# Optimization experiments

Hardware: AMD Instinct MI355X
Metric: run time of the kernel (lower is better)

The kernel has to match this reference:

```python
import jax, jax.numpy as jnp
import numpy as np

BATCH = 2048
N_CHANS = 128
SUBDIM = 64
N_OUT = 4
KARCHER_STEPS = 2
TRACE_EPS = 1e-4
REEIG_THR = 1e-4
BN_EPS = 1e-5
SQRT2 = float(np.sqrt(2.0))


def _sym(X):
    return 0.5 * (X + jnp.swapaxes(X, -1, -2))


def _fapply(X, fn):
    # apply fn to eigenvalues of a batch of symmetric matrices
    w, V = jnp.linalg.eigh(X)
    return jnp.einsum('...ij,...j,...kj->...ik', V, fn(w), V)


def spd_logm(X):
    return _fapply(X, jnp.log)


def spd_expm(X):
    return _fapply(X, jnp.exp)


def spd_powm(X, p):
    return _fapply(X, lambda w: jnp.exp(p * jnp.log(w)))


def setup_inputs() -> dict:
    key = jax.random.key(0)
    k1, k2, k3 = jax.random.split(key, 3)
    # SPD covariance inputs: Wishart-style, eigenvalues distinct a.s.
    A = jax.random.normal(k1, (BATCH, N_CHANS, 2 * N_CHANS), jnp.float32)
    X = A @ jnp.swapaxes(A, -1, -2) / (2 * N_CHANS) + 1e-3 * jnp.eye(N_CHANS, dtype=jnp.float32)
    # BiMap weight: stiefel (semi-orthogonal) init
    W = jnp.linalg.qr(jax.random.normal(k2, (N_CHANS, SUBDIM), jnp.float32))[0]
    L = SUBDIM * (SUBDIM + 1) // 2  # 2080
    Wc = jax.random.normal(k3, (N_OUT, L), jnp.float32) * 0.02
    bc = jnp.zeros((N_OUT,), jnp.float32)
    # BN bias SPD param: near identity but with distinct eigenvalues (keeps eigh grad finite)
    bn_bias = jnp.diag(jnp.linspace(0.9, 1.1, SUBDIM, dtype=jnp.float32))
    return dict(X=X, alpha=jnp.zeros((), jnp.float32), W=W,
                bn_gamma=jnp.ones((), jnp.float32), bn_bias=bn_bias, Wc=Wc, bc=bc)


def reference(X, alpha, W, bn_gamma, bn_bias, Wc, bc):
    n = X.shape[-1]
    I_n = jnp.eye(n, dtype=X.dtype)
    # TraceNorm: normalize to (approximately) unit trace
    tr = jnp.trace(X, axis1=-2, axis2=-1)[:, None, None]
    X = X / (tr + TRACE_EPS)
    # Shrinkage: (1-a) X + a * (tr(X)/n) I, learnable a (init 0)
    mu = jnp.trace(X, axis1=-2, axis2=-1)[:, None, None] / n
    X = (1.0 - alpha) * X + alpha * mu * I_n
    # BiMap: W^T X W  -> (B, d, d)
    X = _sym(jnp.einsum('ji,bjk,kl->bil', W, X, W))
    # ReEig: clamp eigenvalues at threshold
    X = _fapply(X, lambda w: jnp.maximum(w, REEIG_THR))
    # SPDBatchNormMeanVar (training mode, batch stats):
    # Karcher mean G (log-Euclidean init + Karcher flow steps)
    G = spd_expm(jnp.mean(spd_logm(X), axis=0))
    for _ in range(KARCHER_STEPS):
        Gs = spd_powm(G, 0.5)
        Gi = spd_powm(G, -0.5)
        G = Gs @ spd_expm(jnp.mean(spd_logm(_sym(Gi @ X @ Gi)), axis=0)) @ Gs
        G = _sym(G)
    Gi = spd_powm(G, -0.5)
    Lt = spd_logm(_sym(Gi @ X @ Gi))            # tangent vectors at identity
    v = jnp.mean(jnp.sum(Lt * Lt, axis=(-2, -1)))  # batch dispersion
    Y = spd_expm(Lt * (bn_gamma / jnp.sqrt(v + BN_EPS)))
    # affine bias: congruence with SPD bias param
    Bs = spd_powm(_sym(bn_bias), 0.5)
    Y = _sym(Bs @ Y @ Bs)
    # LogEig + upper-triangle vectorization (off-diag * sqrt(2))
    Lg = spd_logm(Y)
    d = Y.shape[-1]
    iu, ju = jnp.triu_indices(d)
    coef = jnp.where(iu == ju, 1.0, SQRT2).astype(X.dtype)
    vec = Lg[:, iu, ju] * coef                   # (B, d(d+1)/2)
    return vec @ Wc.T + bc
```

## Files before the change

kernel.cpp:

```cpp
#include <hip/hip_runtime.h>
#include <math.h>


#define NS_HI   5
#define NSC_IT  12
#define C1      0.0038729833f
#define LNC1    (-5.553730f)
#define SPLIT_S 4096.f
#define SPLIT_R (1.f/4096.f)

typedef _Float16 h16;
typedef _Float16 h16x8 __attribute__((ext_vector_type(8)));
typedef _Float16 h16x4 __attribute__((ext_vector_type(4)));
typedef float    f32x4 __attribute__((ext_vector_type(4)));

#define WS_S1   ((size_t)0)
#define WS_R2   ((size_t)8388608)
#define WS_SM   ((size_t)16777216)
#define SM_LBAR  0
#define SM_EBAR1 4096
#define SM_EBAR2 8192
#define SM_GI0   12288
#define SM_GS0   16384
#define SM_GI1   20480
#define SM_GS1   24576
#define SM_GI2   28672
#define SM_GS2   32768
#define SM_BS    36864
#define SM_VPART 40960
#define SM_S     40992

__device__ __forceinline__ float4 ld4(const float* p){ return *(const float4*)p; }
__device__ __forceinline__ void  st4(float* p, float4 v){ *(float4*)p = v; }

__device__ __forceinline__ int eoff(int r, int c){ return (r*128 + c*2) ^ ((r&7)<<4); }

__device__ __forceinline__ h16x8 frag_ld(const h16* p, int row, int ks, int lg){
  int off = (row*128 + ks*64 + lg*16) ^ ((row&7)<<4);
  return *(const h16x8*)((const char*)p + off);
}
__device__ __forceinline__ h16x8 frag_ld2(const h16* p, int row, int ks, int lg){
  int off = (row*256 + ks*64 + lg*16) ^ ((row&7)<<4);
  return *(const h16x8*)((const char*)p + off);
}
__device__ __forceinline__ h16x4 h4_ld(const h16* p, int r, int c4){
  return *(const h16x4*)((const char*)p + eoff(r,c4));
}
__device__ __forceinline__ void h4_st(h16* p, int r, int c4, h16x4 v){
  *(h16x4*)((char*)p + eoff(r,c4)) = v;
}
__device__ __forceinline__ void split2(float v, h16& h, h16& l){
  h16 hh = (h16)v;
  h = hh;
  l = (h16)((v - (float)hh) * SPLIT_S);
}
__device__ __forceinline__ float join2(h16 h, h16 l){
  return (float)h + (float)l * SPLIT_R;
}

template<int AS,int BS,int GP>
__device__ __forceinline__ void mmT(const h16* Lh,const h16* Ll,
                                    const h16* Rh,const h16* Rl,const h16* gR,
                                    f32x4 acc[2][2], int lane,int wv){
  const int lr=lane&15, lg=lane>>4;
  const int rb=(wv&1)*32, cb=(wv>>1)*32;
  h16x8 ah[2][2], al[2][2];
  #pragma unroll
  for(int rt=0;rt<2;rt++){
    #pragma unroll
    for(int ks=0;ks<2;ks++){
      ah[rt][ks]=frag_ld(Lh, rb+16*rt+lr, ks, lg);
      if(AS) al[rt][ks]=frag_ld(Ll, rb+16*rt+lr, ks, lg);
    }
  }
  f32x4 aM[2][2], aC[2][2];
  const f32x4 vz={0.f,0.f,0.f,0.f};
  #pragma unroll
  for(int rt=0;rt<2;rt++){ aM[rt][0]=vz; aM[rt][1]=vz; aC[rt][0]=vz; aC[rt][1]=vz; }
  #pragma unroll
  for(int ct=0;ct<2;ct++){
    #pragma unroll
    for(int ks=0;ks<2;ks++){
      h16x8 bh, bl;
      if(GP){
        const h16* g = gR + (cb+16*ct+lr)*64 + ks*32 + lg*8;
        bh = *(const h16x8*)g;
        if(BS) bl = *(const h16x8*)(g+4096);
      }else{
        bh = frag_ld(Rh, cb+16*ct+lr, ks, lg);
        if(BS) bl = frag_ld(Rl, cb+16*ct+lr, ks, lg);
      }
      #pragma unroll
      for(int rt=0;rt<2;rt++){
        aM[rt][ct]=__builtin_amdgcn_mfma_f32_16x16x32_f16(ah[rt][ks],bh,aM[rt][ct],0,0,0);
        if(AS) aC[rt][ct]=__builtin_amdgcn_mfma_f32_16x16x32_f16(al[rt][ks],bh,aC[rt][ct],0,0,0);
        if(BS) aC[rt][ct]=__builtin_amdgcn_mfma_f32_16x16x32_f16(ah[rt][ks],bl,aC[rt][ct],0,0,0);
      }
    }
  }
  #pragma unroll
  for(int rt=0;rt<2;rt++)
    #pragma unroll
    for(int ct=0;ct<2;ct++)
      acc[rt][ct] = (AS||BS) ? (aM[rt][ct] + aC[rt][ct]*SPLIT_R) : aM[rt][ct];
}

__device__ __forceinline__ void stS(h16* Dh,h16* Dl,const f32x4 acc[2][2],
                                    const float (*dI)[2][4],
                                    int lane,int wv,float scale,float dadd){
  const int lr=lane&15, lg=lane>>4, rb=(wv&1)*32, cb=(wv>>1)*32;
  #pragma unroll
  for(int rt=0;rt<2;rt++){
    int i0=rb+16*rt+lg*4;
    #pragma unroll
    for(int ct=0;ct<2;ct++){
      int j=cb+16*ct+lr;
      h16x4 h4,l4;
      #pragma unroll
      for(int r=0;r<4;r++){
        float x=fmaf(acc[rt][ct][r],scale, dadd*dI[rt][ct][r]);
        h16 hh,ll; split2(x,hh,ll); h4[r]=hh; l4[r]=ll;
      }
      int off=(j*128+i0*2)^((j&7)<<4);
      *(h16x4*)((char*)Dh+off)=h4;
      *(h16x4*)((char*)Dl+off)=l4;
    }
  }
}
__device__ __forceinline__ void stH(h16* Dh,const f32x4 acc[2][2],
                                    const float (*dI)[2][4],
                                    int lane,int wv,float scale,float dadd){
  const int lr=lane&15, lg=lane>>4, rb=(wv&1)*32, cb=(wv>>1)*32;
  #pragma unroll
  for(int rt=0;rt<2;rt++){
    int i0=rb+16*rt+lg*4;
    #pragma unroll
    for(int ct=0;ct<2;ct++){
      int j=cb+16*ct+lr;
      h16x4 h4;
      #pragma unroll
      for(int r=0;r<4;r++){
        float x=fmaf(acc[rt][ct][r],scale, dadd*dI[rt][ct][r]);
        h4[r]=(h16)x;
      }
      int off=(j*128+i0*2)^((j&7)<<4);
      *(h16x4*)((char*)Dh+off)=h4;
    }
  }
}

__device__ __forceinline__ void st_gl(float* G, const f32x4 acc[2][2],
                                      int lane,int wv,float scale,float dadd){
  const int lr=lane&15, lg=lane>>4, rb=(wv&1)*32, cb=(wv>>1)*32;
  #pragma unroll
  for(int rt=0;rt<2;rt++){
    int i0=rb+16*rt+lg*4;
    #pragma unroll
    for(int ct=0;ct<2;ct++){
      int j=cb+16*ct+lr;
      float4 v; float* vf=(float*)&v;
      #pragma unroll
      for(int r=0;r<4;r++){
        float x=acc[rt][ct][r]*scale;
        if (i0+r==j) x += dadd;
        vf[r]=x;
      }
      st4(G + j*64 + i0, v);
    }
  }
}

__device__ __forceinline__ void st_park(h16* gh, const f32x4 acc[2][2], int lane,int wv){
  const int lr=lane&15, lg=lane>>4, rb=(wv&1)*32, cb=(wv>>1)*32;
  #pragma unroll
  for(int rt=0;rt<2;rt++){
    int i0=rb+16*rt+lg*4;
    #pragma unroll
    for(int ct=0;ct<2;ct++){
      int j=cb+16*ct+lr;
      h16x4 h4,l4;
      #pragma unroll
      for(int r=0;r<4;r++){ h16 hh,ll; split2(acc[rt][ct][r],hh,ll); h4[r]=hh; l4[r]=ll; }
      *(h16x4*)(gh + j*64 + i0) = h4;
      *(h16x4*)(gh + 4096 + j*64 + i0) = l4;
    }
  }
}

__device__ __forceinline__ void snap(const h16* Ph,const h16* Pl,float (*v)[2][4],
                                     int lane,int wv){
  const int lr=lane&15, lg=lane>>4, rb=(wv&1)*32, cb=(wv>>1)*32;
  #pragma unroll
  for(int rt=0;rt<2;rt++){
    int i0=rb+16*rt+lg*4;
    #pragma unroll
    for(int ct=0;ct<2;ct++){
      int j=cb+16*ct+lr;
      h16x4 h=h4_ld(Ph,j,i0), l=h4_ld(Pl,j,i0);
      #pragma unroll
      for(int r=0;r<4;r++) v[rt][ct][r]=join2(h[r],l[r]);
    }
  }
}

__device__ __forceinline__ void fill_gl(h16* Ph, h16* Pl, const float* g,
                                        float scale, float dshift, int tid){
  int r = tid>>2;
  #pragma unroll
  for(int q=0;q<4;q++){
    int c4 = (tid&3)*16 + q*4;
    float4 v = ld4(g + r*64 + c4);
    float vv[4]={v.x,v.y,v.z,v.w};
    h16x4 h4,l4;
    #pragma unroll
    for(int j=0;j<4;j++){
      float x = vv[j];
      if (c4+j == r) x += dshift;
      x *= scale;
      h16 hh,ll; split2(x,hh,ll); h4[j]=hh; l4[j]=ll;
    }
    h4_st(Ph,r,c4,h4); h4_st(Pl,r,c4,l4);
  }
}

__device__ __forceinline__ void plane_out(const h16* Ph, const h16* Pl, float* g,
                                          float scale, int tid){
  int r=tid>>2;
  #pragma unroll
  for(int q=0;q<4;q++){
    int c4=(tid&3)*16+q*4;
    h16x4 h4=h4_ld(Ph,r,c4), l4=h4_ld(Pl,r,c4);
    float4 v;
    v.x=join2(h4[0],l4[0])*scale;
    v.y=join2(h4[1],l4[1])*scale;
    v.z=join2(h4[2],l4[2])*scale;
    v.w=join2(h4[3],l4[3])*scale;
    st4(g + r*64 + c4, v);
  }
}

__device__ __forceinline__ void diag_add(h16* Ph, h16* Pl, float add, int tid){
  if (tid<64){
    int off = (tid*128 + tid*2) ^ ((tid&7)<<4);
    h16* ph = (h16*)((char*)Ph + off);
    h16* pl = (h16*)((char*)Pl + off);
    float v = join2(*ph,*pl) + add;
    h16 hh,ll; split2(v,hh,ll);
    *ph=hh; *pl=ll;
  }
}

__device__ float block_sum(float v, float* red, int tid){
  red[tid]=v; __syncthreads();
  for(int off=128; off>0; off>>=1){
    if (tid<off) red[tid]+=red[tid+off];
    __syncthreads();
  }
  float r=red[0]; __syncthreads();
  return r;
}

__device__ __forceinline__ float cfj(int j, int J){
  return (j<=J)? 1.f/(float)(2*j+1) : 0.f;
}

__device__ void ns_inv3(h16* Ah,h16* Al,h16* Xh,h16* Xl,h16* Th,h16* Tl,
                        float* red,const float (*dI)[2][4],
                        int tid,int lane,int wv,float lminB){
  {
    int row=tid>>2, seg=tid&3;
    float s=0.f;
    #pragma unroll
    for(int q=0;q<4;q++){
      h16x4 h4 = h4_ld(Ah,row,seg*16+q*4);
      #pragma unroll
      for(int j=0;j<4;j++) s += fabsf((float)h4[j]);
    }
    red[tid]=s*1.001f; __syncthreads();
    if((tid&3)==0) red[tid]=red[tid]+red[tid+1]+red[tid+2]+red[tid+3];
    __syncthreads();
    if(tid==0){ float m=0.f; for(int i=0;i<64;i++) m=fmaxf(m,red[4*i]); red[0]=m; }
    __syncthreads();
  }
  float alpha = 2.f/(lminB + red[0]);
  {
    int r=tid>>2;
    h16 ahh,all_; split2(alpha,ahh,all_);
    #pragma unroll
    for(int q=0;q<4;q++){
      int c4=(tid&3)*16+q*4;
      h16x4 h4={(h16)0,(h16)0,(h16)0,(h16)0};
      h16x4 l4={(h16)0,(h16)0,(h16)0,(h16)0};
      #pragma unroll
      for(int j=0;j<4;j++) if (c4+j==r){ h4[j]=ahh; l4[j]=all_; }
      h4_st(Xh,r,c4,h4); h4_st(Xl,r,c4,l4);
    }
  }
  __syncthreads();
  f32x4 acc[2][2];
  for(int it=0;it<NS_HI;it++){
    mmT<0,0,0>(Ah,0,Xh,0,0,acc,lane,wv); __syncthreads();
    stH(Th,acc,dI,lane,wv,-1.f,2.f); __syncthreads();
    mmT<0,0,0>(Xh,0,Th,0,0,acc,lane,wv); __syncthreads();
    stH(Xh,acc,dI,lane,wv,1.f,0.f); __syncthreads();
  }
  mmT<1,0,0>(Ah,Al,Xh,0,0,acc,lane,wv); __syncthreads();
  stS(Th,Tl,acc,dI,lane,wv,-1.f,2.f); __syncthreads();
  mmT<0,1,0>(Xh,0,Th,Tl,0,acc,lane,wv); __syncthreads();
  stS(Xh,Xl,acc,dI,lane,wv,1.f,0.f); __syncthreads();
  mmT<1,1,0>(Ah,Al,Xh,Xl,0,acc,lane,wv); __syncthreads();
  stS(Th,Tl,acc,dI,lane,wv,-1.f,2.f); __syncthreads();
  mmT<1,1,0>(Xh,Xl,Th,Tl,0,acc,lane,wv); __syncthreads();
  stS(Xh,Xl,acc,dI,lane,wv,1.f,0.f); __syncthreads();
}

__device__ void logm3(h16* Ah,h16* Al,h16* Xh,h16* Xl,h16* Th,h16* Tl,
                      h16* parkh, float* red, const float (*dI)[2][4],
                      float cshift,int C,int J,int tid,int lane,int wv,
                      f32x4 accOut[2][2]){
  ns_inv3(Ah,Al,Xh,Xl,Th,Tl,red,dI,tid,lane,wv,cshift);
  diag_add(Ah,Al,-2.f*cshift,tid);
  __syncthreads();
  f32x4 acc[2][2];
  mmT<1,1,0>(Ah,Al,Xh,Xl,0,acc,lane,wv); __syncthreads();
  stS(Th,Tl,acc,dI,lane,wv,1.f,0.f);
  st_park(parkh,acc,lane,wv);
  __syncthreads();
  mmT<1,1,0>(Th,Tl,Th,Tl,0,acc,lane,wv); __syncthreads();
  stS(Ah,Al,acc,dI,lane,wv,1.f,0.f); __syncthreads();
  mmT<1,1,0>(Ah,Al,Ah,Al,0,acc,lane,wv); __syncthreads();
  stS(Xh,Xl,acc,dI,lane,wv,1.f,0.f); __syncthreads();
  float sv[2][2][4], s2v[2][2][4];
  f32x4 accw[2][2];
  mmT<1,1,0>(Xh,Xl,Ah,Al,0,accw,lane,wv);
  snap(Ah,Al,sv,lane,wv);
  snap(Xh,Xl,s2v,lane,wv);
  {
    float a0=cfj(3*C-3,J),a1=cfj(3*C-2,J),a2=cfj(3*C-1,J);
    int r=tid>>2;
    #pragma unroll
    for(int q=0;q<4;q++){
      int c4=(tid&3)*16+q*4;
      h16x4 sh=h4_ld(Ah,r,c4), sl=h4_ld(Al,r,c4);
      h16x4 th=h4_ld(Xh,r,c4), tl=h4_ld(Xl,r,c4);
      h16x4 h4,l4;
      #pragma unroll
      for(int jj=0;jj<4;jj++){
        float v=a1*join2(sh[jj],sl[jj])+a2*join2(th[jj],tl[jj]);
        if(c4+jj==r) v+=a0;
        h16 hh,ll; split2(v,hh,ll); h4[jj]=hh; l4[jj]=ll;
      }
      h4_st(Th,r,c4,h4); h4_st(Tl,r,c4,l4);
    }
  }
  __syncthreads();
  stS(Xh,Xl,accw,dI,lane,wv,1.f,0.f); __syncthreads();
  for(int i=C-2;i>=0;i--){
    mmT<1,1,0>(Th,Tl,Xh,Xl,0,acc,lane,wv);
    float a0=cfj(3*i,J),a1=cfj(3*i+1,J),a2=cfj(3*i+2,J);
    #pragma unroll
    for(int rt=0;rt<2;rt++)
      #pragma unroll
      for(int ct=0;ct<2;ct++)
        #pragma unroll
        for(int r=0;r<4;r++)
          acc[rt][ct][r]+=a0*dI[rt][ct][r]+a1*sv[rt][ct][r]+a2*s2v[rt][ct][r];
    __syncthreads();
    stS(Th,Tl,acc,dI,lane,wv,1.f,0.f);
    __syncthreads();
  }
  mmT<1,1,1>(Th,Tl,(const h16*)0,(const h16*)0,parkh,accOut,lane,wv);
}

__device__ void exp3(h16* Lh,h16* Ll, h16* Bh,h16* Bl, h16* Ph,h16* Pl,
                     const float (*dI)[2][4], float s,
                     int tid,int lane,int wv){
  f32x4 acc[2][2];
  mmT<1,1,0>(Lh,Ll,Lh,Ll,0,acc,lane,wv); __syncthreads();
  stS(Bh,Bl,acc,dI,lane,wv,1.f,0.f); __syncthreads();
  float lv[2][2][4], l2v[2][2][4];
  snap(Lh,Ll,lv,lane,wv);
  snap(Bh,Bl,l2v,lane,wv);
  float aj[15]; aj[0]=1.f;
  #pragma unroll
  for(int j=1;j<15;j++) aj[j]=aj[j-1]*s/(float)j;
  {
    int r=tid>>2;
    #pragma unroll
    for(int q=0;q<4;q++){
      int c4=(tid&3)*16+q*4;
      h16x4 sh=h4_ld(Lh,r,c4), sl=h4_ld(Ll,r,c4);
      h16x4 th=h4_ld(Bh,r,c4), tl=h4_ld(Bl,r,c4);
      h16x4 h4,l4;
      #pragma unroll
      for(int jj=0;jj<4;jj++){
        float v = aj[13]*join2(sh[jj],sl[jj]) + aj[14]*join2(th[jj],tl[jj]);
        if (c4+jj==r) v+=aj[12];
        h16 hh,ll; split2(v,hh,ll); h4[jj]=hh; l4[jj]=ll;
      }
      h4_st(Ph,r,c4,h4); h4_st(Pl,r,c4,l4);
    }
  }
  __syncthreads();
  mmT<1,1,0>(Bh,Bl,Lh,Ll,0,acc,lane,wv); __syncthreads();
  stS(Bh,Bl,acc,dI,lane,wv,1.f,0.f); __syncthreads();
  #pragma unroll
  for(int i=3;i>=0;i--){
    mmT<1,1,0>(Ph,Pl,Bh,Bl,0,acc,lane,wv);
    #pragma unroll
    for(int rt=0;rt<2;rt++)
      #pragma unroll
      for(int ct=0;ct<2;ct++)
        #pragma unroll
        for(int r=0;r<4;r++)
          acc[rt][ct][r]+=aj[3*i]*dI[rt][ct][r]+aj[3*i+1]*lv[rt][ct][r]+aj[3*i+2]*l2v[rt][ct][r];
    __syncthreads();
    stS(Ph,Pl,acc,dI,lane,wv,1.f,0.f);
    __syncthreads();
  }
}

__device__ void ns_sqrt3(h16* Yh,h16* Yl,h16* Zh,h16* Zl,h16* Th,h16* Tl,
                         const float (*dI)[2][4], int tid,int lane,int wv){
  {
    int r=tid>>2;
    h16 oh,ol; split2(1.f,oh,ol);
    #pragma unroll
    for(int q=0;q<4;q++){
      int c4=(tid&3)*16+q*4;
      h16x4 h4={(h16)0,(h16)0,(h16)0,(h16)0};
      h16x4 l4={(h16)0,(h16)0,(h16)0,(h16)0};
      #pragma unroll
      for(int j=0;j<4;j++) if (c4+j==r){ h4[j]=oh; l4[j]=ol; }
      h4_st(Zh,r,c4,h4); h4_st(Zl,r,c4,l4);
    }
  }
  __syncthreads();
  f32x4 aY[2][2], aZ[2][2];
  for(int it=0; it<NSC_IT; it++){
    mmT<1,1,0>(Zh,Zl,Yh,Yl,0,aY,lane,wv); __syncthreads();
    stS(Th,Tl,aY,dI,lane,wv,-0.5f,1.5f); __syncthreads();
    mmT<1,1,0>(Yh,Yl,Th,Tl,0,aY,lane,wv);
    mmT<1,1,0>(Th,Tl,Zh,Zl,0,aZ,lane,wv);
    __syncthreads();
    stS(Yh,Yl,aY,dI,lane,wv,1.f,0.f);
    stS(Zh,Zl,aZ,dI,lane,wv,1.f,0.f);
    __syncthreads();
  }
}

#define DECL_DI(dIname) \
  float dIname[2][2][4]; \
  { int rb_=(wv&1)*32, cb_=(wv>>1)*32; \
    _Pragma("unroll") \
    for(int rt=0;rt<2;rt++) \
      _Pragma("unroll") \
      for(int ct=0;ct<2;ct++) \
        _Pragma("unroll") \
        for(int r=0;r<4;r++) \
          dIname[rt][ct][r]=((rb_+16*rt+(lane>>4)*4+r)==(cb_+16*ct+(lane&15)))?1.f:0.f; }


__global__ __launch_bounds__(256) void kA(const float* __restrict__ Xg, const float* alphaP,
    const float* __restrict__ Wg, float* S1g, float* R2){
  __shared__ __align__(16) char lds[65536];
  int tid=threadIdx.x, b=blockIdx.x, lane=tid&63, wv=tid>>6;
  int lr=lane&15, lg=lane>>4;
  DECL_DI(dI);
  const float* Xb = Xg + (size_t)b*16384;
  h16* Wph=(h16*)lds;         h16* Wpl=Wph+8192;
  h16* Tph=(h16*)(lds+32768); h16* Tpl=Tph+8192;
  {
    int k0=tid>>1, nh=(tid&1)*32;
    const float* wr = Wg + k0*64 + nh;
    #pragma unroll
    for(int q=0;q<8;q++){
      float4 u=ld4(wr+q*4);
      float uu[4]={u.x,u.y,u.z,u.w};
      #pragma unroll
      for(int j=0;j<4;j++){
        int n=nh+q*4+j;
        h16 hh,ll; split2(uu[j],hh,ll);
        int off=(n*256+k0*2)^((n&7)<<4);
        *(h16*)((char*)Wph+off)=hh;
        *(h16*)((char*)Wpl+off)=ll;
      }
    }
  }
  float tv=(tid<128)? Xb[tid*129]:0.f;
  float tr=block_sum(tv,(float*)(lds+32768),tid);
  float al=alphaP[0];
  float f1=1.f/(tr+1e-4f);
  float scl=(1.f-al)*f1;
  float shift=al*(tr*f1)*(1.f/128.f);
  f32x4 aM[2][4], aC[2][4];
  const f32x4 vz={0.f,0.f,0.f,0.f};
  #pragma unroll
  for(int rt=0;rt<2;rt++)
    #pragma unroll
    for(int ct=0;ct<4;ct++){ aM[rt][ct]=vz; aC[rt][ct]=vz; }
  int mb=wv*32;
  for(int ks=0;ks<4;ks++){
    h16x8 xah[2], xal[2];
    #pragma unroll
    for(int rt=0;rt<2;rt++){
      const float* px=Xb+(size_t)(mb+16*rt+lr)*128+ks*32+lg*8;
      float4 u0=ld4(px), u1=ld4(px+4);
      float uv[8]={u0.x,u0.y,u0.z,u0.w,u1.x,u1.y,u1.z,u1.w};
      #pragma unroll
      for(int e=0;e<8;e++){ h16 hh,ll; split2(uv[e],hh,ll); xah[rt][e]=hh; xal[rt][e]=ll; }
    }
    #pragma unroll
    for(int ct=0;ct<4;ct++){
      h16x8 bh=frag_ld2(Wph,ct*16+lr,ks,lg);
      h16x8 bl=frag_ld2(Wpl,ct*16+lr,ks,lg);
      #pragma unroll
      for(int rt=0;rt<2;rt++){
        aM[rt][ct]=__builtin_amdgcn_mfma_f32_16x16x32_f16(xah[rt],bh,aM[rt][ct],0,0,0);
        aC[rt][ct]=__builtin_amdgcn_mfma_f32_16x16x32_f16(xal[rt],bh,aC[rt][ct],0,0,0);
        aC[rt][ct]=__builtin_amdgcn_mfma_f32_16x16x32_f16(xah[rt],bl,aC[rt][ct],0,0,0);
      }
    }
  }
  __syncthreads();
  #pragma unroll
  for(int rt=0;rt<2;rt++){
    int i0=mb+16*rt+lg*4;
    #pragma unroll
    for(int ct=0;ct<4;ct++){
      int j=ct*16+lr;
      h16x4 h4,l4;
      #pragma unroll
      for(int r=0;r<4;r++){
        float x=aM[rt][ct][r]+aC[rt][ct][r]*SPLIT_R;
        h16 hh,ll; split2(x,hh,ll); h4[r]=hh; l4[r]=ll;
      }
      int off=(j*256+i0*2)^((j&7)<<4);
      *(h16x4*)((char*)Tph+off)=h4;
      *(h16x4*)((char*)Tpl+off)=l4;
    }
  }
  __syncthreads();
  f32x4 sM[2][2], sC[2][2];
  #pragma unroll
  for(int rt=0;rt<2;rt++){ sM[rt][0]=vz; sM[rt][1]=vz; sC[rt][0]=vz; sC[rt][1]=vz; }
  int rb=(wv&1)*32, cb=(wv>>1)*32;
  for(int ks=0;ks<4;ks++){
    h16x8 ah2[2], al2[2];
    #pragma unroll
    for(int rt=0;rt<2;rt++){
      ah2[rt]=frag_ld2(Wph,rb+16*rt+lr,ks,lg);
      al2[rt]=frag_ld2(Wpl,rb+16*rt+lr,ks,lg);
    }
    #pragma unroll
    for(int ct=0;ct<2;ct++){
      h16x8 bh=frag_ld2(Tph,cb+16*ct+lr,ks,lg);
      h16x8 bl=frag_ld2(Tpl,cb+16*ct+lr,ks,lg);
      #pragma unroll
      for(int rt=0;rt<2;rt++){
        sM[rt][ct]=__builtin_amdgcn_mfma_f32_16x16x32_f16(ah2[rt],bh,sM[rt][ct],0,0,0);
        sC[rt][ct]=__builtin_amdgcn_mfma_f32_16x16x32_f16(al2[rt],bh,sC[rt][ct],0,0,0);
        sC[rt][ct]=__builtin_amdgcn_mfma_f32_16x16x32_f16(ah2[rt],bl,sC[rt][ct],0,0,0);
      }
    }
  }
  f32x4 accS[2][2];
  #pragma unroll
  for(int rt=0;rt<2;rt++)
    #pragma unroll
    for(int ct=0;ct<2;ct++) accS[rt][ct]=sM[rt][ct]+sC[rt][ct]*SPLIT_R;
  __syncthreads();
  st_gl(S1g+(size_t)b*4096, accS, lane,wv, scl, shift);
  h16* Ah=(h16*)lds;          h16* Al=Ah+4096;
  h16* Xh=(h16*)(lds+16384);  h16* Xl=Xh+4096;
  h16* Th=(h16*)(lds+32768);  h16* Tl=Th+4096;
  float* red=(float*)(lds+49152);
  stS(Ah,Al,accS,dI,lane,wv, scl, shift + C1);
  __syncthreads();
  f32x4 aL[2][2];
  h16* parkh=(h16*)(R2+(size_t)b*4096);
  logm3(Ah,Al,Xh,Xl,Th,Tl,parkh,red,dI, C1, 11, 30, tid,lane,wv, aL);
  __syncthreads();
  st_gl(R2+(size_t)b*4096, aL, lane,wv, 2.f, LNC1);
}

__global__ __launch_bounds__(256) void kRed(const float* __restrict__ R2, float* outM, float scale){
  __shared__ float red[256];
  int tid=threadIdx.x; int ee=tid&31; int sl=tid>>5;
  int e0 = blockIdx.x*32 + ee;
  float s=0.f;
  for(int j=0;j<256;j++) s += R2[(size_t)(sl+8*j)*4096 + e0];
  red[tid]=s; __syncthreads();
  if (sl<4) red[tid]+=red[tid+128];
  __syncthreads();
  if (sl<2) red[tid]+=red[tid+64];
  __syncthreads();
  if (sl==0) outM[e0] = (red[tid]+red[tid+32])*scale;
}

__global__ __launch_bounds__(256) void kB(const float* Lbar, const float* biasP,
     float* Gi0, float* Gs0, float* Bs){
  __shared__ __align__(16) char lds[50176];
  int tid=threadIdx.x, lane=tid&63, wv=tid>>6;
  DECL_DI(dI);
  h16* s0h=(h16*)lds;          h16* s0l=s0h+4096;
  h16* s1h=(h16*)(lds+16384);  h16* s1l=s1h+4096;
  h16* s2h=(h16*)(lds+32768);  h16* s2l=s2h+4096;
  float* red=(float*)(lds+49152);
  float tr = block_sum((tid<64)? Lbar[tid*65]:0.f, red, tid);
  float cb_ = tr*(1.f/64.f);
  fill_gl(s0h,s0l, Lbar, 0.5f, -cb_, tid);
  __syncthreads();
  exp3(s0h,s0l,s1h,s1l,s2h,s2l, dI, 1.f, tid,lane,wv);
  plane_out(s2h,s2l, Gs0, expf(0.5f*cb_), tid);
  __syncthreads();
  exp3(s0h,s0l,s1h,s1l,s2h,s2l, dI, -1.f, tid,lane,wv);
  plane_out(s2h,s2l, Gi0, expf(-0.5f*cb_), tid);
  __syncthreads();
  float tb = block_sum((tid<64)? biasP[tid*65]:0.f, red, tid);
  float itb=1.f/tb;
  {
    int r=tid>>2;
    #pragma unroll
    for(int q=0;q<4;q++){
      int c4=(tid&3)*16+q*4;
      float4 v=ld4(biasP + r*64 + c4);
      float vv[4]={v.x,v.y,v.z,v.w};
      h16x4 h4,l4;
      #pragma unroll
      for(int j=0;j<4;j++){
        float x = 0.5f*(vv[j] + biasP[(c4+j)*64 + r]) * itb;
        h16 hh,ll; split2(x,hh,ll); h4[j]=hh; l4[j]=ll;
      }
      h4_st(s0h,r,c4,h4); h4_st(s0l,r,c4,l4);
    }
  }
  __syncthreads();
  ns_sqrt3(s0h,s0l,s1h,s1l,s2h,s2l, dI, tid,lane,wv);
  plane_out(s0h,s0l, Bs, sqrtf(tb), tid);
}

__global__ __launch_bounds__(256,3) void kC(const float* __restrict__ S1g, const float* GiP,
     float* R2, float* vpart, int doV){
  __shared__ __align__(16) char lds[50176];
  int tid=threadIdx.x, b=blockIdx.x, lane=tid&63, wv=tid>>6;
  DECL_DI(dI);
  h16* s0h=(h16*)lds;          h16* s0l=s0h+4096;
  h16* s1h=(h16*)(lds+16384);  h16* s1l=s1h+4096;
  h16* s2h=(h16*)(lds+32768);  h16* s2l=s2h+4096;
  float* red=(float*)(lds+49152);
  fill_gl(s0h,s0l, S1g+(size_t)b*4096, 1.f,0.f, tid);
  fill_gl(s1h,s1l, GiP, 1.f,0.f, tid);
  __syncthreads();
  f32x4 acc[2][2];
  mmT<1,1,0>(s0h,s0l,s1h,s1l,0,acc,lane,wv); __syncthreads();
  stS(s2h,s2l,acc,dI,lane,wv,1.f,0.f); __syncthreads();
  mmT<1,1,0>(s1h,s1l,s2h,s2l,0,acc,lane,wv); __syncthreads();
  stS(s0h,s0l,acc,dI,lane,wv,1.f,1.f); __syncthreads();
  f32x4 aL[2][2];
  h16* parkh=(h16*)(R2+(size_t)b*4096);
  logm3(s0h,s0l,s1h,s1l,s2h,s2l,parkh,red,dI, 1.f, 11, 30, tid,lane,wv, aL);
  __syncthreads();
  st_gl(R2+(size_t)b*4096, aL, lane,wv, 2.f, 0.f);
  if (doV){
    float s=0.f;
    #pragma unroll
    for(int rt=0;rt<2;rt++)
      #pragma unroll
      for(int ct=0;ct<2;ct++)
        #pragma unroll
        for(int r=0;r<4;r++){ float lv=2.f*aL[rt][ct][r]; s=fmaf(lv,lv,s); }
    __syncthreads();
    s = block_sum(s, red, tid);
    if (tid==0) atomicAdd(vpart + (b&31), s);
  }
}

__global__ __launch_bounds__(256) void kD(const float* Ebar, const float* GsP,
     float* GsN, float* GiN){
  __shared__ __align__(16) char lds[50176];
  int tid=threadIdx.x, lane=tid&63, wv=tid>>6;
  DECL_DI(dI);
  h16* s0h=(h16*)lds;          h16* s0l=s0h+4096;
  h16* s1h=(h16*)(lds+16384);  h16* s1l=s1h+4096;
  h16* s2h=(h16*)(lds+32768);  h16* s2l=s2h+4096;
  float* red=(float*)(lds+49152);
  fill_gl(s0h,s0l, Ebar, 1.f,0.f, tid); __syncthreads();
  exp3(s0h,s0l,s1h,s1l,s2h,s2l, dI, 1.f, tid,lane,wv);
  fill_gl(s0h,s0l, GsP, 1.f,0.f, tid);
  __syncthreads();
  f32x4 acc[2][2];
  mmT<1,1,0>(s2h,s2l,s0h,s0l,0,acc,lane,wv); __syncthreads();
  stS(s1h,s1l,acc,dI,lane,wv,1.f,0.f); __syncthreads();
  mmT<1,1,0>(s0h,s0l,s1h,s1l,0,acc,lane,wv);
  float tv=0.f;
  #pragma unroll
  for(int rt=0;rt<2;rt++)
    #pragma unroll
    for(int ct=0;ct<2;ct++)
      #pragma unroll
      for(int r=0;r<4;r++) tv += acc[rt][ct][r]*dI[rt][ct][r];
  float t = block_sum(tv, red, tid);
  stS(s0h,s0l,acc,dI,lane,wv,1.f/t,0.f); __syncthreads();
  ns_sqrt3(s0h,s0l,s1h,s1l,s2h,s2l, dI, tid,lane,wv);
  float st_=sqrtf(t), ist=1.f/st_;
  plane_out(s0h,s0l, GsN, st_, tid);
  plane_out(s1h,s1l, GiN, ist, tid);
}

__global__ void kF2(const float* vpart, const float* gammaP, float* sOut){
  if (threadIdx.x==0 && blockIdx.x==0){
    float v=0.f;
    for(int i=0;i<32;i++) v+=vpart[i];
    v *= (1.f/2048.f);
    sOut[0] = gammaP[0] / sqrtf(v + 1e-5f);
  }
}

__global__ __launch_bounds__(256,3) void kG(float* R2, const float* BsP, const float* sP,
     const float* __restrict__ WcP, const float* bcP, float* outP){
  __shared__ __align__(16) char lds[50176];
  int tid=threadIdx.x, b=blockIdx.x, lane=tid&63, wv=tid>>6;
  DECL_DI(dI);
  h16* s0h=(h16*)lds;          h16* s0l=s0h+4096;
  h16* s1h=(h16*)(lds+16384);  h16* s1l=s1h+4096;
  h16* s2h=(h16*)(lds+32768);  h16* s2l=s2h+4096;
  float* red=(float*)(lds+49152);
  fill_gl(s0h,s0l, R2+(size_t)b*4096, 1.f,0.f, tid); __syncthreads();
  float s = sP[0];
  exp3(s0h,s0l,s1h,s1l,s2h,s2l, dI, s, tid,lane,wv);
  fill_gl(s0h,s0l, BsP, 1.f,0.f, tid);
  __syncthreads();
  f32x4 acc[2][2];
  mmT<1,1,0>(s2h,s2l,s0h,s0l,0,acc,lane,wv); __syncthreads();
  stS(s1h,s1l,acc,dI,lane,wv,1.f,0.f); __syncthreads();
  mmT<1,1,0>(s0h,s0l,s1h,s1l,0,acc,lane,wv); __syncthreads();
  stS(s2h,s2l,acc,dI,lane,wv,1.f,1.f); __syncthreads();
  f32x4 aL[2][2];
  h16* parkh=(h16*)(R2+(size_t)b*4096);
  logm3(s2h,s2l,s0h,s0l,s1h,s1l,parkh,red,dI, 1.f, 6, 15, tid,lane,wv, aL);
  float o0=0,o1=0,o2=0,o3=0;
  {
    int lr=lane&15, lq=lane>>4, rb=(wv&1)*32, cb=(wv>>1)*32;
    #pragma unroll
    for(int rt=0;rt<2;rt++)
      #pragma unroll
      for(int ct=0;ct<2;ct++)
        #pragma unroll
        for(int r=0;r<4;r++){
          int i=rb+16*rt+lq*4+r, j=cb+16*ct+lr;
          float lg2=2.f*aL[rt][ct][r];
          int a=(i<j)? i:j, bb=(i<j)? j:i;
          int tri = a*64 - ((a*(a-1))>>1) + (bb-a);
          float w = (i==j)? lg2 : lg2*0.70710678118654752f;
          o0=fmaf(w, WcP[tri],      o0);
          o1=fmaf(w, WcP[2080+tri], o1);
          o2=fmaf(w, WcP[4160+tri], o2);
          o3=fmaf(w, WcP[6240+tri], o3);
        }
  }
  __syncthreads();
  float* redv=(float*)lds;
  float4 pk; pk.x=o0; pk.y=o1; pk.z=o2; pk.w=o3;
  st4(redv+4*tid, pk); __syncthreads();
  for(int off=128; off>0; off>>=1){
    if (tid<off){
      float4 x=ld4(redv+4*tid), y=ld4(redv+4*(tid+off));
      x.x+=y.x; x.y+=y.y; x.z+=y.z; x.w+=y.w;
      st4(redv+4*tid, x);
    }
    __syncthreads();
  }
  if (tid==0){
    outP[b*4+0]=redv[0]+bcP[0];
    outP[b*4+1]=redv[1]+bcP[1];
    outP[b*4+2]=redv[2]+bcP[2];
    outP[b*4+3]=redv[3]+bcP[3];
  }
}

extern "C" void kernel_launch(void* const* d_in, const int* in_sizes, int n_in,
                              void* d_out, int out_size, void* d_ws, size_t ws_size,
                              hipStream_t stream){
  const float* X     = (const float*)d_in[0];
  const float* alpha = (const float*)d_in[1];
  const float* W     = (const float*)d_in[2];
  const float* gamma = (const float*)d_in[3];
  const float* bias  = (const float*)d_in[4];
  const float* Wc    = (const float*)d_in[5];
  const float* bc    = (const float*)d_in[6];
  float* ws = (float*)d_ws;
  float* S1 = ws + WS_S1;
  float* R2 = ws + WS_R2;
  float* sm = ws + WS_SM;

  hipMemsetAsync(sm + SM_VPART, 0, 33*sizeof(float), stream);

  kA  <<<2048,256,0,stream>>>(X, alpha, W, S1, R2);
  kRed<<<128, 256,0,stream>>>(R2, sm+SM_LBAR, 1.f/2048.f);
  kB  <<<1,   256,0,stream>>>(sm+SM_LBAR, bias, sm+SM_GI0, sm+SM_GS0, sm+SM_BS);
  kC  <<<2048,256,0,stream>>>(S1, sm+SM_GI0, R2, nullptr, 0);
  kRed<<<128, 256,0,stream>>>(R2, sm+SM_EBAR1, 1.f/2048.f);
  kD  <<<1,   256,0,stream>>>(sm+SM_EBAR1, sm+SM_GS0, sm+SM_GS1, sm+SM_GI1);
  kC  <<<2048,256,0,stream>>>(S1, sm+SM_GI1, R2, nullptr, 0);
  kRed<<<128, 256,0,stream>>>(R2, sm+SM_EBAR2, 1.f/2048.f);
  kD  <<<1,   256,0,stream>>>(sm+SM_EBAR2, sm+SM_GS1, sm+SM_GS2, sm+SM_GI2);
  kC  <<<2048,256,0,stream>>>(S1, sm+SM_GI2, R2, sm+SM_VPART, 1);
  kF2 <<<1,1,0,stream>>>(sm+SM_VPART, gamma, sm+SM_S);
  kG  <<<2048,256,0,stream>>>(R2, sm+SM_BS, sm+SM_S, Wc, bc, (float*)d_out);
}
```

Before: 923.1 us.

## Restructure matrix log/exp polynomial evaluation with degree-4 Paterson-Stockmeyer and ping-pong buffers

Replaces the degree-3 block Horner evaluation in the matrix logarithm with a degree-4 Paterson-Stockmeyer scheme that uses register-held powers. The series term counts are retuned per call site (fewer Chebyshev/atanh terms for the first logm), and the final Newton-Schulz refinement step is dropped in one case. Ping-pong LDS buffers let one barrier per step be removed in the Newton-Schulz and Horner loops, and the high-precision low halves of the early Newton-Schulz iterates are no longer kept. exp is restructured the same way, and the inverse exponential is computed from a negated input. The aim is fewer matmuls and fewer syncs, at the risk of reduced accuracy from the shorter series and the skipped refinement.

```diff
diff --git a/kernel.cpp b/kernel.cpp
--- a/kernel.cpp
+++ b/kernel.cpp
@@ -2,7 +2,6 @@
 #include <math.h>
 
 
-#define NS_HI   5
 #define NSC_IT  12
 #define C1      0.0038729833f
 #define LNC1    (-5.553730f)
@@ -203,6 +202,40 @@
   }
 }
 
+__device__ __forceinline__ void snapa(float (*v)[2][4], const f32x4 acc[2][2]){
+  #pragma unroll
+  for(int rt=0;rt<2;rt++)
+    #pragma unroll
+    for(int ct=0;ct<2;ct++)
+      #pragma unroll
+      for(int r=0;r<4;r++) v[rt][ct][r]=acc[rt][ct][r];
+}
+
+__device__ __forceinline__ void addK4(f32x4 acc[2][2], const float (*dI)[2][4],
+    const float (*sv)[2][4], const float (*s2v)[2][4], const float (*s3v)[2][4],
+    float a0,float a1,float a2,float a3){
+  #pragma unroll
+  for(int rt=0;rt<2;rt++)
+    #pragma unroll
+    for(int ct=0;ct<2;ct++)
+      #pragma unroll
+      for(int r=0;r<4;r++)
+        acc[rt][ct][r] += a0*dI[rt][ct][r] + a1*sv[rt][ct][r]
+                        + a2*s2v[rt][ct][r] + a3*s3v[rt][ct][r];
+}
+
+__device__ __forceinline__ void addK3(f32x4 acc[2][2], const float (*dI)[2][4],
+    const float (*lv)[2][4], const float (*l2v)[2][4],
+    float a0,float a1,float a2){
+  #pragma unroll
+  for(int rt=0;rt<2;rt++)
+    #pragma unroll
+    for(int ct=0;ct<2;ct++)
+      #pragma unroll
+      for(int r=0;r<4;r++)
+        acc[rt][ct][r] += a0*dI[rt][ct][r] + a1*lv[rt][ct][r] + a2*l2v[rt][ct][r];
+}
+
 __device__ __forceinline__ void fill_gl(h16* Ph, h16* Pl, const float* g,
                                         float scale, float dshift, int tid){
   int r = tid>>2;
@@ -264,9 +297,10 @@
   return (j<=J)? 1.f/(float)(2*j+1) : 0.f;
 }
 
-__device__ void ns_inv3(h16* Ah,h16* Al,h16* Xh,h16* Xl,h16* Th,h16* Tl,
+template<int NSS>
+__device__ void ns_inv4(h16* Ah,h16* Al,h16* Xh,h16* Xl,h16* Th,h16* Tl,
                         float* red,const float (*dI)[2][4],
-                        int tid,int lane,int wv,float lminB){
+                        int tid,int lane,int wv,float lminB,float postshift){
   {
     int row=tid>>2, seg=tid&3;
     float s=0.f;
@@ -285,137 +319,124 @@
   float alpha = 2.f/(lminB + red[0]);
   {
     int r=tid>>2;
-    h16 ahh,all_; split2(alpha,ahh,all_);
+    h16 ahh=(h16)alpha;
     #pragma unroll
     for(int q=0;q<4;q++){
       int c4=(tid&3)*16+q*4;
       h16x4 h4={(h16)0,(h16)0,(h16)0,(h16)0};
-      h16x4 l4={(h16)0,(h16)0,(h16)0,(h16)0};
-      #pragma unroll
-      for(int j=0;j<4;j++) if (c4+j==r){ h4[j]=ahh; l4[j]=all_; }
-      h4_st(Xh,r,c4,h4); h4_st(Xl,r,c4,l4);
+      #pragma unroll
+      for(int j=0;j<4;j++) if (c4+j==r) h4[j]=ahh;
+      h4_st(Xh,r,c4,h4);
     }
   }
   __syncthreads();
   f32x4 acc[2][2];
-  for(int it=0;it<NS_HI;it++){
-    mmT<0,0,0>(Ah,0,Xh,0,0,acc,lane,wv); __syncthreads();
-    stH(Th,acc,dI,lane,wv,-1.f,2.f); __syncthreads();
-    mmT<0,0,0>(Xh,0,Th,0,0,acc,lane,wv); __syncthreads();
-    stH(Xh,acc,dI,lane,wv,1.f,0.f); __syncthreads();
-  }
-  mmT<1,0,0>(Ah,Al,Xh,0,0,acc,lane,wv); __syncthreads();
+  #pragma unroll
+  for(int it=0;it<5;it++){
+    const h16* Xa=(it&1)?Xl:Xh;
+    h16* Ta=(it&1)?Tl:Th;
+    h16* Xn=(it&1)?Xh:Xl;
+    mmT<0,0,0>(Ah,0,Xa,0,0,acc,lane,wv);
+    stH(Ta,acc,dI,lane,wv,-1.f,2.f); __syncthreads();
+    mmT<0,0,0>(Xa,0,Ta,0,0,acc,lane,wv);
+    stH(Xn,acc,dI,lane,wv,1.f,0.f); __syncthreads();
+  }
+  mmT<1,0,0>(Ah,Al,Xl,0,0,acc,lane,wv);
   stS(Th,Tl,acc,dI,lane,wv,-1.f,2.f); __syncthreads();
-  mmT<0,1,0>(Xh,0,Th,Tl,0,acc,lane,wv); __syncthreads();
-  stS(Xh,Xl,acc,dI,lane,wv,1.f,0.f); __syncthreads();
-  mmT<1,1,0>(Ah,Al,Xh,Xl,0,acc,lane,wv); __syncthreads();
-  stS(Th,Tl,acc,dI,lane,wv,-1.f,2.f); __syncthreads();
-  mmT<1,1,0>(Xh,Xl,Th,Tl,0,acc,lane,wv); __syncthreads();
-  stS(Xh,Xl,acc,dI,lane,wv,1.f,0.f); __syncthreads();
-}
-
-__device__ void logm3(h16* Ah,h16* Al,h16* Xh,h16* Xl,h16* Th,h16* Tl,
+  mmT<0,1,0>(Xl,0,Th,Tl,0,acc,lane,wv); __syncthreads();
+  if(NSS>1){
+    stS(Xh,Xl,acc,dI,lane,wv,1.f,0.f); __syncthreads();
+    mmT<1,1,0>(Ah,Al,Xh,Xl,0,acc,lane,wv);
+    stS(Th,Tl,acc,dI,lane,wv,-1.f,2.f); __syncthreads();
+    mmT<1,1,0>(Xh,Xl,Th,Tl,0,acc,lane,wv); __syncthreads();
+  }
+  stS(Xh,Xl,acc,dI,lane,wv,1.f,0.f);
+  diag_add(Ah,Al,postshift,tid);
+  __syncthreads();
+}
+
+template<int C,int J,int NSS>
+__device__ void logm4(h16* Ah,h16* Al,h16* Xh,h16* Xl,h16* Th,h16* Tl,
                       h16* parkh, float* red, const float (*dI)[2][4],
-                      float cshift,int C,int J,int tid,int lane,int wv,
+                      float cshift,int tid,int lane,int wv,
                       f32x4 accOut[2][2]){
-  ns_inv3(Ah,Al,Xh,Xl,Th,Tl,red,dI,tid,lane,wv,cshift);
-  diag_add(Ah,Al,-2.f*cshift,tid);
-  __syncthreads();
+  ns_inv4<NSS>(Ah,Al,Xh,Xl,Th,Tl,red,dI,tid,lane,wv,cshift,-2.f*cshift);
   f32x4 acc[2][2];
-  mmT<1,1,0>(Ah,Al,Xh,Xl,0,acc,lane,wv); __syncthreads();
+  mmT<1,1,0>(Ah,Al,Xh,Xl,0,acc,lane,wv);
   stS(Th,Tl,acc,dI,lane,wv,1.f,0.f);
   st_park(parkh,acc,lane,wv);
   __syncthreads();
-  mmT<1,1,0>(Th,Tl,Th,Tl,0,acc,lane,wv); __syncthreads();
+  float sv[2][2][4], s2v[2][2][4], s3v[2][2][4];
+  mmT<1,1,0>(Th,Tl,Th,Tl,0,acc,lane,wv);
+  snapa(sv,acc);
   stS(Ah,Al,acc,dI,lane,wv,1.f,0.f); __syncthreads();
-  mmT<1,1,0>(Ah,Al,Ah,Al,0,acc,lane,wv); __syncthreads();
+  mmT<1,1,0>(Ah,Al,Ah,Al,0,acc,lane,wv);
+  snapa(s2v,acc);
   stS(Xh,Xl,acc,dI,lane,wv,1.f,0.f); __syncthreads();
-  float sv[2][2][4], s2v[2][2][4];
-  f32x4 accw[2][2];
-  mmT<1,1,0>(Xh,Xl,Ah,Al,0,accw,lane,wv);
-  snap(Ah,Al,sv,lane,wv);
-  snap(Xh,Xl,s2v,lane,wv);
+  mmT<1,1,0>(Xh,Xl,Ah,Al,0,acc,lane,wv);
+  snapa(s3v,acc);
+  stS(Th,Tl,acc,dI,lane,wv,1.f,0.f); __syncthreads();
+  mmT<1,1,0>(Xh,Xl,Xh,Xl,0,acc,lane,wv);
+  stS(Ah,Al,acc,dI,lane,wv,1.f,0.f);
   {
-    float a0=cfj(3*C-3,J),a1=cfj(3*C-2,J),a2=cfj(3*C-1,J);
-    int r=tid>>2;
-    #pragma unroll
-    for(int q=0;q<4;q++){
-      int c4=(tid&3)*16+q*4;
-      h16x4 sh=h4_ld(Ah,r,c4), sl=h4_ld(Al,r,c4);
-      h16x4 th=h4_ld(Xh,r,c4), tl=h4_ld(Xl,r,c4);
-      h16x4 h4,l4;
-      #pragma unroll
-      for(int jj=0;jj<4;jj++){
-        float v=a1*join2(sh[jj],sl[jj])+a2*join2(th[jj],tl[jj]);
-        if(c4+jj==r) v+=a0;
-        h16 hh,ll; split2(v,hh,ll); h4[jj]=hh; l4[jj]=ll;
-      }
-      h4_st(Th,r,c4,h4); h4_st(Tl,r,c4,l4);
-    }
-  }
-  __syncthreads();
-  stS(Xh,Xl,accw,dI,lane,wv,1.f,0.f); __syncthreads();
-  for(int i=C-2;i>=0;i--){
-    mmT<1,1,0>(Th,Tl,Xh,Xl,0,acc,lane,wv);
-    float a0=cfj(3*i,J),a1=cfj(3*i+1,J),a2=cfj(3*i+2,J);
+    f32x4 p[2][2];
+    float a0=cfj(4*(C-1),J),a1=cfj(4*(C-1)+1,J),a2=cfj(4*(C-1)+2,J),a3=cfj(4*(C-1)+3,J);
     #pragma unroll
     for(int rt=0;rt<2;rt++)
       #pragma unroll
       for(int ct=0;ct<2;ct++)
         #pragma unroll
         for(int r=0;r<4;r++)
-          acc[rt][ct][r]+=a0*dI[rt][ct][r]+a1*sv[rt][ct][r]+a2*s2v[rt][ct][r];
+          p[rt][ct][r]=a0*dI[rt][ct][r]+a1*sv[rt][ct][r]+a2*s2v[rt][ct][r]+a3*s3v[rt][ct][r];
+    stS(Th,Tl,p,dI,lane,wv,1.f,0.f);
+  }
+  __syncthreads();
+  #pragma unroll
+  for(int k=0;k<C-1;k++){
+    int i=C-2-k;
+    const h16 *Ph=(k&1)?Xh:Th; const h16 *Pl=(k&1)?Xl:Tl;
+    h16 *Qh=(k&1)?Th:Xh; h16 *Ql=(k&1)?Tl:Xl;
+    mmT<1,1,0>(Ph,Pl,Ah,Al,0,acc,lane,wv);
+    addK4(acc,dI,sv,s2v,s3v,cfj(4*i,J),cfj(4*i+1,J),cfj(4*i+2,J),cfj(4*i+3,J));
+    stS(Qh,Ql,acc,dI,lane,wv,1.f,0.f);
     __syncthreads();
-    stS(Th,Tl,acc,dI,lane,wv,1.f,0.f);
-    __syncthreads();
-  }
-  mmT<1,1,1>(Th,Tl,(const h16*)0,(const h16*)0,parkh,accOut,lane,wv);
-}
-
-__device__ void exp3(h16* Lh,h16* Ll, h16* Bh,h16* Bl, h16* Ph,h16* Pl,
-                     const float (*dI)[2][4], float s,
-                     int tid,int lane,int wv){
-  f32x4 acc[2][2];
-  mmT<1,1,0>(Lh,Ll,Lh,Ll,0,acc,lane,wv); __syncthreads();
-  stS(Bh,Bl,acc,dI,lane,wv,1.f,0.f); __syncthreads();
+  }
+  mmT<1,1,1>(Xh,Xl,(const h16*)0,(const h16*)0,parkh,accOut,lane,wv);
+}
+
+__device__ void exp4(h16* Lh,h16* Ll, h16* Bh,h16* Bl, h16* Wh,h16* Wl,
+                     const float (*dI)[2][4], float s, int tid,int lane,int wv){
+  float aj[15]; aj[0]=1.f;
+  #pragma unroll
+  for(int j=1;j<15;j++) aj[j]=aj[j-1]*s/(float)j;
   float lv[2][2][4], l2v[2][2][4];
   snap(Lh,Ll,lv,lane,wv);
-  snap(Bh,Bl,l2v,lane,wv);
-  float aj[15]; aj[0]=1.f;
-  #pragma unroll
-  for(int j=1;j<15;j++) aj[j]=aj[j-1]*s/(float)j;
+  f32x4 acc[2][2];
+  mmT<1,1,0>(Lh,Ll,Lh,Ll,0,acc,lane,wv);
+  snapa(l2v,acc);
+  stS(Bh,Bl,acc,dI,lane,wv,1.f,0.f); __syncthreads();
+  mmT<1,1,0>(Bh,Bl,Lh,Ll,0,acc,lane,wv);
+  stS(Wh,Wl,acc,dI,lane,wv,1.f,0.f); __syncthreads();
   {
-    int r=tid>>2;
-    #pragma unroll
-    for(int q=0;q<4;q++){
-      int c4=(tid&3)*16+q*4;
-      h16x4 sh=h4_ld(Lh,r,c4), sl=h4_ld(Ll,r,c4);
-      h16x4 th=h4_ld(Bh,r,c4), tl=h4_ld(Bl,r,c4);
-      h16x4 h4,l4;
-      #pragma unroll
-      for(int jj=0;jj<4;jj++){
-        float v = aj[13]*join2(sh[jj],sl[jj]) + aj[14]*join2(th[jj],tl[jj]);
-        if (c4+jj==r) v+=aj[12];
-        h16 hh,ll; split2(v,hh,ll); h4[jj]=hh; l4[jj]=ll;
-      }
-      h4_st(Ph,r,c4,h4); h4_st(Pl,r,c4,l4);
-    }
-  }
-  __syncthreads();
-  mmT<1,1,0>(Bh,Bl,Lh,Ll,0,acc,lane,wv); __syncthreads();
-  stS(Bh,Bl,acc,dI,lane,wv,1.f,0.f); __syncthreads();
-  #pragma unroll
-  for(int i=3;i>=0;i--){
-    mmT<1,1,0>(Ph,Pl,Bh,Bl,0,acc,lane,wv);
+    f32x4 p[2][2];
     #pragma unroll
     for(int rt=0;rt<2;rt++)
       #pragma unroll
       for(int ct=0;ct<2;ct++)
         #pragma unroll
         for(int r=0;r<4;r++)
-          acc[rt][ct][r]+=aj[3*i]*dI[rt][ct][r]+aj[3*i+1]*lv[rt][ct][r]+aj[3*i+2]*l2v[rt][ct][r];
-    __syncthreads();
-    stS(Ph,Pl,acc,dI,lane,wv,1.f,0.f);
+          p[rt][ct][r]=aj[12]*dI[rt][ct][r]+aj[13]*lv[rt][ct][r]+aj[14]*l2v[rt][ct][r];
+    stS(Lh,Ll,p,dI,lane,wv,1.f,0.f);
+  }
+  __syncthreads();
+  #pragma unroll
+  for(int k=0;k<4;k++){
+    int i=3-k;
+    const h16 *Ph=(k&1)?Bh:Lh; const h16 *Pl=(k&1)?Bl:Ll;
+    h16 *Qh=(k&1)?Lh:Bh; h16 *Ql=(k&1)?Ll:Bl;
+    mmT<1,1,0>(Ph,Pl,Wh,Wl,0,acc,lane,wv);
+    addK3(acc,dI,lv,l2v,aj[3*i],aj[3*i+1],aj[3*i+2]);
+    stS(Qh,Ql,acc,dI,lane,wv,1.f,0.f);
     __syncthreads();
   }
 }
@@ -579,7 +600,7 @@
   __syncthreads();
   f32x4 aL[2][2];
   h16* parkh=(h16*)(R2+(size_t)b*4096);
-  logm3(Ah,Al,Xh,Xl,Th,Tl,parkh,red,dI, C1, 11, 30, tid,lane,wv, aL);
+  logm4<4,15,1>(Ah,Al,Xh,Xl,Th,Tl,parkh,red,dI, C1, tid,lane,wv, aL);
   __syncthreads();
   st_gl(R2+(size_t)b*4096, aL, lane,wv, 2.f, LNC1);
 }
@@ -611,11 +632,13 @@
   float cb_ = tr*(1.f/64.f);
   fill_gl(s0h,s0l, Lbar, 0.5f, -cb_, tid);
   __syncthreads();
-  exp3(s0h,s0l,s1h,s1l,s2h,s2l, dI, 1.f, tid,lane,wv);
-  plane_out(s2h,s2l, Gs0, expf(0.5f*cb_), tid);
-  __syncthreads();
-  exp3(s0h,s0l,s1h,s1l,s2h,s2l, dI, -1.f, tid,lane,wv);
-  plane_out(s2h,s2l, Gi0, expf(-0.5f*cb_), tid);
+  exp4(s0h,s0l,s1h,s1l,s2h,s2l, dI, 1.f, tid,lane,wv);
+  plane_out(s0h,s0l, Gs0, expf(0.5f*cb_), tid);
+  __syncthreads();
+  fill_gl(s0h,s0l, Lbar, -0.5f, -cb_, tid);
+  __syncthreads();
+  exp4(s0h,s0l,s1h,s1l,s2h,s2l, dI, 1.f, tid,lane,wv);
+  plane_out(s0h,s0l, Gi0, expf(-0.5f*cb_), tid);
   __syncthreads();
   float tb = block_sum((tid<64)? biasP[tid*65]:0.f, red, tid);
   float itb=1.f/tb;
@@ -653,13 +676,13 @@
   fill_gl(s1h,s1l, GiP, 1.f,0.f, tid);
   __syncthreads();
   f32x4 acc[2][2];
-  mmT<1,1,0>(s0h,s0l,s1h,s1l,0,acc,lane,wv); __syncthreads();
+  mmT<1,1,0>(s0h,s0l,s1h,s1l,0,acc,lane,wv);
   stS(s2h,s2l,acc,dI,lane,wv,1.f,0.f); __syncthreads();
-  mmT<1,1,0>(s1h,s1l,s2h,s2l,0,acc,lane,wv); __syncthreads();
+  mmT<1,1,0>(s1h,s1l,s2h,s2l,0,acc,lane,wv);
   stS(s0h,s0l,acc,dI,lane,wv,1.f,1.f); __syncthreads();
   f32x4 aL[2][2];
   h16* parkh=(h16*)(R2+(size_t)b*4096);
-  logm3(s0h,s0l,s1h,s1l,s2h,s2l,parkh,red,dI, 1.f, 11, 30, tid,lane,wv, aL);
+  logm4<8,30,2>(s0h,s0l,s1h,s1l,s2h,s2l,parkh,red,dI, 1.f, tid,lane,wv, aL);
   __syncthreads();
   st_gl(R2+(size_t)b*4096, aL, lane,wv, 2.f, 0.f);
   if (doV){
@@ -686,13 +709,13 @@
   h16* s2h=(h16*)(lds+32768);  h16* s2l=s2h+4096;
   float* red=(float*)(lds+49152);
   fill_gl(s0h,s0l, Ebar, 1.f,0.f, tid); __syncthreads();
-  exp3(s0h,s0l,s1h,s1l,s2h,s2l, dI, 1.f, tid,lane,wv);
-  fill_gl(s0h,s0l, GsP, 1.f,0.f, tid);
+  exp4(s0h,s0l,s1h,s1l,s2h,s2l, dI, 1.f, tid,lane,wv);
+  fill_gl(s1h,s1l, GsP, 1.f,0.f, tid);
   __syncthreads();
   f32x4 acc[2][2];
-  mmT<1,1,0>(s2h,s2l,s0h,s0l,0,acc,lane,wv); __syncthreads();
-  stS(s1h,s1l,acc,dI,lane,wv,1.f,0.f); __syncthreads();
   mmT<1,1,0>(s0h,s0l,s1h,s1l,0,acc,lane,wv);
+  stS(s2h,s2l,acc,dI,lane,wv,1.f,0.f); __syncthreads();
+  mmT<1,1,0>(s1h,s1l,s2h,s2l,0,acc,lane,wv);
   float tv=0.f;
   #pragma unroll
   for(int rt=0;rt<2;rt++)
@@ -728,17 +751,17 @@
   float* red=(float*)(lds+49152);
   fill_gl(s0h,s0l, R2+(size_t)b*4096, 1.f,0.f, tid); __syncthreads();
   float s = sP[0];
-  exp3(s0h,s0l,s1h,s1l,s2h,s2l, dI, s, tid,lane,wv);
-  fill_gl(s0h,s0l, BsP, 1.f,0.f, tid);
+  exp4(s0h,s0l,s1h,s1l,s2h,s2l, dI, s, tid,lane,wv);
+  fill_gl(s1h,s1l, BsP, 1.f,0.f, tid);
   __syncthreads();
   f32x4 acc[2][2];
-  mmT<1,1,0>(s2h,s2l,s0h,s0l,0,acc,lane,wv); __syncthreads();
-  stS(s1h,s1l,acc,dI,lane,wv,1.f,0.f); __syncthreads();
-  mmT<1,1,0>(s0h,s0l,s1h,s1l,0,acc,lane,wv); __syncthreads();
-  stS(s2h,s2l,acc,dI,lane,wv,1.f,1.f); __syncthreads();
+  mmT<1,1,0>(s0h,s0l,s1h,s1l,0,acc,lane,wv);
+  stS(s2h,s2l,acc,dI,lane,wv,1.f,0.f); __syncthreads();
+  mmT<1,1,0>(s1h,s1l,s2h,s2l,0,acc,lane,wv);
+  stS(s0h,s0l,acc,dI,lane,wv,1.f,1.f); __syncthreads();
   f32x4 aL[2][2];
   h16* parkh=(h16*)(R2+(size_t)b*4096);
-  logm3(s2h,s2l,s0h,s0l,s1h,s1l,parkh,red,dI, 1.f, 6, 15, tid,lane,wv, aL);
+  logm4<4,15,2>(s0h,s0l,s1h,s1l,s2h,s2l,parkh,red,dI, 1.f, tid,lane,wv, aL);
   float o0=0,o1=0,o2=0,o3=0;
   {
     int lr=lane&15, lq=lane>>4, rb=(wv&1)*32, cb=(wv>>1)*32;
```

Measured after the change: 778.8 us. 15.6% less time.
